# Performance work log

Measured on AMD Instinct MI355X. Metric: run time of the kernel, lower is better.

The kernel has to match this reference:

```python
import jax, jax.numpy as jnp
import numpy as np
import math


def ste_round(x):
    # round with straight-through gradient (identity in bwd)
    return x + jax.lax.stop_gradient(jnp.round(x) - x)


def ste_floor(x):
    return x + jax.lax.stop_gradient(jnp.floor(x) - x)


def _conv(x, w, b):
    # 5x5 stride-2 conv, padding=2 (kernel_size//2), NCHW/OIHW
    y = jax.lax.conv_general_dilated(
        x, w, window_strides=(2, 2), padding=[(2, 2), (2, 2)],
        dimension_numbers=('NCHW', 'OIHW', 'NCHW'))
    return y + b[None, :, None, None]


def _split_conv(x, w, b_int, mul, split=4):
    # 4 redundant sub-convolutions with floor-STE quantized integer weights/biases
    wq = ste_round(w)  # wSTE: round-to-int with STE
    out = 0.0
    for i in range(split):
        out = out + _conv(x, ste_floor((wq + i) / split), ste_floor((b_int + i) / split))
    return out * mul[None, :, None, None]


def _forward(x, w0, b0, w1, b1, w2, b2, w3, b3, mul0, mul1, mul2, mul3,
             relu0, relu1, relu2, md0, md1, md2, md3, ga_left):
    Bits = 8; clp_k = 8; in_scale = 8; scl_k = 3
    relus = [relu0, relu1, relu2]
    clp = [round((2 ** Bits - 1) / r * 2 ** (16 + clp_k)) for r in relus]
    scl = [math.floor((r + 2 ** (scl_k - 1)) / 2 ** scl_k) for r in relus]

    # quantize input to uint8 range
    x = jnp.clip(ste_round(x * 2 ** in_scale), 0, 255)

    # ---- layer 0 ----
    x = _split_conv(x, w0, ste_round(b0 * 2 ** in_scale), mul0)
    x = ste_floor((x + 2.0 ** (md0 - 1 + in_scale - clp_k)) / 2.0 ** (md0 + in_scale - clp_k))
    x = jnp.clip(x, 0, clp[0])
    x = ste_floor((ste_round(x * scl[0]) + 2.0 ** (15 + clp_k - scl_k)) / 2.0 ** (16 + clp_k - scl_k))

    # ---- layers 1, 2 ----
    for w_, b_, mul_, md_, idx in ((w1, b1, mul1, md1, 1), (w2, b2, mul2, md2, 2)):
        x = _split_conv(x, w_, ste_round(b_), mul_)
        x = ste_floor((x + 2.0 ** (md_ - 1 - clp_k)) / 2.0 ** (md_ - clp_k))
        x = jnp.clip(x, 0, clp[idx])
        x = ste_floor((ste_round(x * scl[idx]) + 2.0 ** (15 + clp_k - scl_k)) / 2.0 ** (16 + clp_k - scl_k))

    # ---- layer 3 (latent) ----
    x = _split_conv(x, w3, ste_round(b3), mul3)
    x = ste_floor((x + 2.0 ** (md3 - 1 - ga_left)) / 2.0 ** (md3 - ga_left))
    return x


def setup_inputs():
    key = jax.random.key(0)
    ks = jax.random.split(key, 16)
    N, M = 192, 320
    d = {}
    d['x'] = jax.random.uniform(ks[0], (4, 3, 512, 512), dtype=jnp.float32)
    # float weights whose round() gives small ints (integerized LIC weights)
    d['w0'] = jax.random.normal(ks[1], (N, 3, 5, 5), dtype=jnp.float32) * 3.0
    d['b0'] = jax.random.normal(ks[2], (N,), dtype=jnp.float32)
    d['w1'] = jax.random.normal(ks[3], (N, N, 5, 5), dtype=jnp.float32) * 3.0
    d['b1'] = jax.random.normal(ks[4], (N,), dtype=jnp.float32) * 16.0
    d['w2'] = jax.random.normal(ks[5], (N, N, 5, 5), dtype=jnp.float32) * 3.0
    d['b2'] = jax.random.normal(ks[6], (N,), dtype=jnp.float32) * 16.0
    d['w3'] = jax.random.normal(ks[7], (M, N, 5, 5), dtype=jnp.float32) * 3.0
    d['b3'] = jax.random.normal(ks[8], (M,), dtype=jnp.float32) * 16.0
    # per-channel integer-valued fixed-point multipliers
    d['mul0'] = jax.random.randint(ks[9], (N,), 1, 64).astype(jnp.float32)
    d['mul1'] = jax.random.randint(ks[10], (N,), 1, 64).astype(jnp.float32)
    d['mul2'] = jax.random.randint(ks[11], (N,), 1, 64).astype(jnp.float32)
    d['mul3'] = jax.random.randint(ks[12], (M,), 1, 64).astype(jnp.float32)
    d['relu0'] = 65536; d['relu1'] = 65536; d['relu2'] = 65536
    d['md0'] = 7; d['md1'] = 15; d['md2'] = 15; d['md3'] = 10
    d['ga_left'] = 4
    return d


def reference(x, w0, b0, w1, b1, w2, b2, w3, b3, mul0, mul1, mul2, mul3,
              relu0, relu1, relu2, md0, md1, md2, md3, ga_left):
    return _forward(x, w0, b0, w1, b1, w2, b2, w3, b3, mul0, mul1, mul2, mul3,
                    relu0, relu1, relu2, md0, md1, md2, md3, ga_left)
```

## Files before the change

### kernel.cpp

```cpp
#include <hip/hip_runtime.h>
#include <hip/hip_bf16.h>

typedef int i32x4 __attribute__((ext_vector_type(4)));
typedef unsigned int u32;
typedef unsigned long long u64;
typedef long long ll;

__device__ __forceinline__ void load_lds16(const void* g, void* l) {
  __builtin_amdgcn_global_load_lds(
      (const __attribute__((address_space(1))) u32*)g,
      (__attribute__((address_space(3))) u32*)l, 16, 0, 0);
}

template <int MF>
__device__ __forceinline__ void pack_i8(int j, const float* wsrc, signed char* wdst) {
  int e = j & 15, col = (j >> 4) & 15, q = (j >> 8) & 3, t = j >> 10;
  int mf = t % MF; t /= MF; int ch = t % 3; int tap = t / 3;
  int oc = mf * 16 + col, ci = ch * 64 + q * 16 + e;
  wdst[j] = (signed char)(int)rintf(wsrc[(oc * 192 + ci) * 25 + tap]);
}

__global__ __launch_bounds__(256) void prep_all(
    const float* __restrict__ w0, const float* __restrict__ w1,
    const float* __restrict__ w2, const float* __restrict__ w3,
    signed char* __restrict__ w0q, signed char* __restrict__ w1p,
    signed char* __restrict__ w2p, signed char* __restrict__ w3p,
    signed char* __restrict__ zbuf,
    int* __restrict__ totw0, int* __restrict__ totw1,
    int* __restrict__ totw2, int* __restrict__ totw3)
{
  const int blk = blockIdx.x;
  const int tid = threadIdx.x;

  if (blk < 2048) {
    if (blk == 0 && tid < 128)
      ((unsigned long long*)zbuf)[tid] = 0x8080808080808080ULL;
    const int R0 = 24576;
    const int R1 = 921600;
    const int R3 = 1536000;
    const int total = R0 + 2 * R1 + R3;
    for (int i = blk * 256 + tid; i < total; i += 2048 * 256) {
      if (i < R0) {
        int e = i & 15, colA = (i >> 4) & 15, q = (i >> 8) & 3, t = i >> 10;
        int mf = t % 12, ch = t / 12;
        signed char v = 0;
        if (e < 15 && (ch == 0 || q == 0)) {
          int ky = (ch == 0) ? q : 4;
          int ci = e / 5, kx = e - ci * 5;
          v = (signed char)(int)rintf(
              w0[((mf * 16 + colA) * 3 + ci) * 25 + ky * 5 + kx]);
        }
        w0q[i] = v;
      } else if (i < R0 + R1) {
        pack_i8<12>(i - R0, w1, w1p);
      } else if (i < R0 + 2 * R1) {
        pack_i8<12>(i - R0 - R1, w2, w2p);
      } else {
        pack_i8<20>(i - R0 - 2 * R1, w3, w3p);
      }
    }
  } else {
    int t = (blk - 2048) * 256 + tid;
    if (t < 704 * 16) {
      int oc = t >> 4, q = t & 15;
      const float* ws; int* tot; int o = oc;
      if (oc < 192)      { ws = w1; tot = totw1; }
      else if (oc < 384) { ws = w2; tot = totw2; o = oc - 192; }
      else               { ws = w3; tot = totw3; o = oc - 384; }
      const float* p = ws + (size_t)o * 4800 + q * 300;
      int s = 0;
      #pragma unroll 4
      for (int j = 0; j < 300; j++) s += (int)rintf(p[j]);
      atomicAdd(&tot[o], s);
    } else {
      int oc = t - 704 * 16;
      if (oc < 192) {
        const float* p = w0 + (size_t)oc * 75;
        int s = 0;
        #pragma unroll 5
        for (int j = 0; j < 75; j++) s += (int)rintf(p[j]);
        totw0[oc] = s;
      }
    }
  }
}

__global__ __launch_bounds__(192, 3) void conv0F(
    const float* __restrict__ x, const signed char* __restrict__ wq,
    const float* __restrict__ bias, const float* __restrict__ mulv,
    const int* __restrict__ totw,
    const int* __restrict__ reluP, const int* __restrict__ mdP,
    unsigned char* __restrict__ outA)
{
  __shared__ signed char ilds[3][5][132];

  const int tid = threadIdx.x;
  const int lane = tid & 63;
  const int col = lane & 15;
  const int quad = lane >> 4;
  const int w = tid >> 6;
  const int blk = blockIdx.x;
  const int oxblk = blk & 3;
  const int oy = (blk >> 2) & 255;
  const int b = blk >> 10;
  const int oxbase = oxblk * 64;

  i32x4 afr[2][4];
  #pragma unroll
  for (int ch = 0; ch < 2; ch++)
    #pragma unroll
    for (int i = 0; i < 4; i++)
      afr[ch][i] = *(const i32x4*)(wq + ch * 12288 + (w * 4 + i) * 1024 + lane * 16);

  const float* xb = x + (size_t)b * 3 * 512 * 512;
  for (int i = tid; i < 990; i += 192) {
    int j = i % 66; int t = i / 66; int r = t % 5; int ci = t / 5;
    int iy = 2 * oy - 2 + r;
    int ix = 2 * oxbase - 2 + 2 * j;
    int v0 = -128, v1 = -128;
    if ((unsigned)iy < 512u) {
      const float* row = xb + ((size_t)ci * 512 + iy) * 512;
      if ((unsigned)ix < 512u) {
        float xv = rintf(row[ix] * 256.0f);
        v0 = (int)fminf(fmaxf(xv, 0.0f), 255.0f) - 128;
      }
      if ((unsigned)(ix + 1) < 512u) {
        float xv = rintf(row[ix + 1] * 256.0f);
        v1 = (int)fminf(fmaxf(xv, 0.0f), 255.0f) - 128;
      }
    }
    *(unsigned short*)&ilds[ci][r][2 * j] =
        (unsigned short)((v0 & 0xFF) | ((v1 & 0xFF) << 8));
  }
  __syncthreads();

  i32x4 acc[4][4];
  #pragma unroll
  for (int fm = 0; fm < 4; fm++)
    #pragma unroll
    for (int fn = 0; fn < 4; fn++) acc[fm][fn] = (i32x4){0, 0, 0, 0};

  #pragma unroll
  for (int ch = 0; ch < 2; ch++) {
    const int row = (ch == 0) ? quad : 4;
    i32x4 bfr[4];
    #pragma unroll
    for (int fn = 0; fn < 4; fn++) {
      const int xb2 = 2 * (fn * 16 + col);
      const int o8 = (xb2 & 3) * 8;
      const int ab = xb2 & ~3;
      u64 w0_, w1_, w2_;
      {
        const u32* p0 = (const u32*)&ilds[0][row][ab];
        const u32* p1 = (const u32*)&ilds[1][row][ab];
        const u32* p2 = (const u32*)&ilds[2][row][ab];
        w0_ = (u64)p0[0] | ((u64)p0[1] << 32);
        w1_ = (u64)p1[0] | ((u64)p1[1] << 32);
        w2_ = (u64)p2[0] | ((u64)p2[1] << 32);
      }
      u32 a0 = (u32)(w0_ >> o8);
      u32 a1 = ((u32)(w0_ >> (o8 + 32)) & 0xFFu) | (((u32)(w1_ >> o8)) << 8);
      u32 a2 = ((u32)(w1_ >> (o8 + 24)) & 0xFFFFu) | (((u32)(w2_ >> o8)) << 16);
      u32 a3 = (u32)(w2_ >> (o8 + 16));
      bfr[fn] = (i32x4){(int)a0, (int)a1, (int)a2, (int)a3};
    }
    #pragma unroll
    for (int fm = 0; fm < 4; fm++)
      #pragma unroll
      for (int fn = 0; fn < 4; fn++)
        acc[fm][fn] = __builtin_amdgcn_mfma_i32_16x16x64_i8(
            afr[ch][fm], bfr[fn], acc[fm][fn], 0, 0, 0);
  }

  const size_t pix0 = ((size_t)(b * 256 + oy)) * 256 + oxbase;
  const int rl = reluP[0];
  const int sh = mdP[0];
  const ll clpv_ll = llrint(255.0 / (double)rl * 16777216.0);
  const int clpv = clpv_ll > 0x7FFFFFFFLL ? 0x7FFFFFFF : (int)clpv_ll;
  const int sclv = (int)((rl + 4) >> 3);
  const int rnd = 1 << (sh - 1);
  #pragma unroll
  for (int fm = 0; fm < 4; fm++) {
    const int oc0 = w * 64 + fm * 16 + quad * 4;
    int bim[4], mu32[4];
    #pragma unroll
    for (int r = 0; r < 4; r++) {
      int bi = (int)llrintf(bias[oc0 + r] * 256.0f) + 128 * totw[oc0 + r];
      mu32[r] = (int)llrintf(mulv[oc0 + r]);
      bim[r] = bi * mu32[r];
    }
    #pragma unroll
    for (int fn = 0; fn < 4; fn++) {
      const size_t pix = pix0 + fn * 16 + col;
      u32 wd = 0;
      #pragma unroll
      for (int r = 0; r < 4; r++) {
        int vi = acc[fm][fn][r] * mu32[r] + bim[r];
        int y = (vi + rnd) >> sh;
        y = y < 0 ? 0 : (y > clpv ? clpv : y);
        y = (y * sclv + (1 << 20)) >> 21;
        wd |= (((u32)y ^ 0x80u) & 0xFFu) << (8 * r);
      }
      *(u32*)(outA + pix * 192 + oc0) = wd;
    }
  }
}

template <int COUT, int HIN, int WIN, int HOUT, int WOUT, int MW,
          int KSPLIT, bool DIRECT>
__global__ __launch_bounds__(MW * 64, 3) void convS(
    const signed char* __restrict__ act, const signed char* __restrict__ wp,
    const float* __restrict__ bias, const float* __restrict__ mulv,
    const int* __restrict__ totw,
    const int* __restrict__ reluP, const int* __restrict__ mdP,
    const signed char* __restrict__ zbuf,
    unsigned char* __restrict__ outA, int* __restrict__ outP)
{
  constexpr int CIN = 192;
  constexpr int PASSES = 4;
  constexpr int MAXP = (PASSES + MW - 1) / MW;
  constexpr int SAe = MW * 4096;
  constexpr int TX = WOUT / 16;
  constexpr int TYB = HOUT / 4;
  constexpr int TPP = 25 / KSPLIT;
  constexpr int NSTEP = TPP * 3;
  constexpr int PSZ = 4 * HOUT * WOUT * COUT;
  static_assert(MW * 64 == COUT, "M covers COUT");

  __shared__ __align__(16) char smem[2 * 4096];

  const int tid = threadIdx.x;
  const int lane = tid & 63;
  const int col = lane & 15;
  const int quad = lane >> 4;
  const int w = tid >> 6;
  const int part = blockIdx.y;

  int bx = blockIdx.x;
  const int tx = bx % TX; bx /= TX;
  const int ty = bx % TYB;
  const int b = bx / TYB;
  const int ox0 = tx * 16;
  const int oy0 = ty * 4;

  const signed char* bptr[MAXP];
  int bmx[MAXP], bmy[MAXP];
  #pragma unroll
  for (int k = 0; k < MAXP; k++) {
    int p = w + k * MW;
    if (p >= PASSES) break;
    int oxv = ox0 + col;
    int oyv = oy0 + p;
    bptr[k] = act + ((size_t)b * HIN * WIN + (size_t)(2 * oyv) * WIN + 2 * oxv) * CIN
              + quad * 16;
    int mx = 0, my = 0;
    #pragma unroll
    for (int kk = 0; kk < 5; kk++) {
      if ((unsigned)(2 * oxv + kk - 2) < (unsigned)WIN) mx |= 1 << kk;
      if ((unsigned)(2 * oyv + kk - 2) < (unsigned)HIN) my |= 1 << kk;
    }
    bmx[k] = mx; bmy[k] = my;
  }

  auto stageStep = [&](int tap, int ch, int sel) {
    const int ky = tap / 5, kx = tap % 5;
    const int offB = ((ky - 2) * WIN + (kx - 2)) * CIN + ch * 64;
    #pragma unroll
    for (int k = 0; k < MAXP; k++) {
      int p = w + k * MW;
      if (p >= PASSES) break;
      bool v = ((bmx[k] >> kx) & 1) && ((bmy[k] >> ky) & 1);
      const signed char* g = v ? (bptr[k] + offB) : (zbuf + quad * 16);
      load_lds16(g, smem + sel * 4096 + p * 1024);
    }
  };

  i32x4 acc[4][4];
  #pragma unroll
  for (int fm = 0; fm < 4; fm++)
    #pragma unroll
    for (int fn = 0; fn < 4; fn++) acc[fm][fn] = (i32x4){0, 0, 0, 0};

  const int tap0 = part * TPP;
  stageStep(tap0, 0, 0);
  const signed char* aptr = wp + (size_t)(tap0 * 3) * SAe + w * 4096 + lane * 16;
  i32x4 afn[4];
  #pragma unroll
  for (int i = 0; i < 4; i++)
    afn[i] = *(const i32x4*)(aptr + i * 1024);

  int tapN = tap0, chN = 1;

  #pragma unroll 1
  for (int sl = 0; sl < NSTEP; sl++) {
    __syncthreads();

    if (sl + 1 < NSTEP) {
      stageStep(tapN, chN, (sl + 1) & 1);
      chN++;
      if (chN == 3) { chN = 0; tapN++; }
    }

    i32x4 afc[4];
    #pragma unroll
    for (int i = 0; i < 4; i++) afc[i] = afn[i];
    if (sl + 1 < NSTEP) {
      aptr += SAe;
      #pragma unroll
      for (int i = 0; i < 4; i++)
        afn[i] = *(const i32x4*)(aptr + i * 1024);
    }

    const char* pB = smem + (sl & 1) * 4096 + lane * 16;
    i32x4 bfr[4];
    #pragma unroll
    for (int i = 0; i < 4; i++)
      bfr[i] = *(const i32x4*)(pB + i * 1024);
    #pragma unroll
    for (int fm = 0; fm < 4; fm++)
      #pragma unroll
      for (int fn = 0; fn < 4; fn++)
        acc[fm][fn] = __builtin_amdgcn_mfma_i32_16x16x64_i8(
            afc[fm], bfr[fn], acc[fm][fn], 0, 0, 0);
  }

  if constexpr (DIRECT) {
    const int rl = reluP[0];
    const int sh = mdP[0] - 8;
    const ll clpv = llrint(255.0 / (double)rl * 16777216.0);
    const ll sclv = (ll)((rl + 4) >> 3);
    #pragma unroll
    for (int fm = 0; fm < 4; fm++) {
      const int oc0 = w * 64 + fm * 16 + quad * 4;
      ll bi[4], mu[4];
      #pragma unroll
      for (int r = 0; r < 4; r++) {
        bi[r] = llrintf(bias[oc0 + r]) + 128LL * totw[oc0 + r];
        mu[r] = llrintf(mulv[oc0 + r]);
      }
      #pragma unroll
      for (int fn = 0; fn < 4; fn++) {
        const int oyv = oy0 + fn;
        const int oxv = ox0 + col;
        u32 wd = 0;
        #pragma unroll
        for (int r = 0; r < 4; r++) {
          ll vi = ((ll)acc[fm][fn][r] + bi[r]) * mu[r];
          ll y = (vi + (1LL << (sh - 1))) >> sh;
          y = y < 0 ? 0LL : (y > clpv ? clpv : y);
          y = (y * sclv + (1LL << 20)) >> 21;
          wd |= (((u32)y ^ 0x80u) & 0xFFu) << (8 * r);
        }
        *(u32*)(outA + ((size_t)((b * HOUT + oyv) * WOUT + oxv)) * COUT + oc0) = wd;
      }
    }
  } else {
    int* pout = outP + (size_t)part * PSZ;
    #pragma unroll
    for (int fm = 0; fm < 4; fm++) {
      const int oc0 = w * 64 + fm * 16 + quad * 4;
      #pragma unroll
      for (int fn = 0; fn < 4; fn++) {
        const int oyv = oy0 + fn;
        const int oxv = ox0 + col;
        *(i32x4*)(pout + ((size_t)((b * HOUT + oyv) * WOUT + oxv)) * COUT + oc0) =
            acc[fm][fn];
      }
    }
  }
}

__global__ __launch_bounds__(256) void reduce2(
    const int* __restrict__ partP, const float* __restrict__ bias,
    const float* __restrict__ mulv, const int* __restrict__ totw,
    const int* __restrict__ reluP, const int* __restrict__ mdP,
    unsigned char* __restrict__ outA)
{
  const int gid = blockIdx.x * 256 + threadIdx.x;
  const int PSZ4 = 4 * 64 * 64 * 192 / 4;
  const int4* pp = (const int4*)partP;
  int4 sv = pp[gid];
  #pragma unroll
  for (int p = 1; p < 5; p++) {
    int4 v = pp[(size_t)p * PSZ4 + gid];
    sv.x += v.x; sv.y += v.y; sv.z += v.z; sv.w += v.w;
  }
  int sa[4] = {sv.x, sv.y, sv.z, sv.w};
  const int oc0 = (gid * 4) % 192;
  const int rl = reluP[0];
  const int sh = mdP[0] - 8;
  const ll clpv = llrint(255.0 / (double)rl * 16777216.0);
  const ll sclv = (ll)((rl + 4) >> 3);
  u32 wd = 0;
  #pragma unroll
  for (int r = 0; r < 4; r++) {
    ll bi = llrintf(bias[oc0 + r]) + 128LL * totw[oc0 + r];
    ll mu = llrintf(mulv[oc0 + r]);
    ll vi = ((ll)sa[r] + bi) * mu;
    ll y = (vi + (1LL << (sh - 1))) >> sh;
    y = y < 0 ? 0LL : (y > clpv ? clpv : y);
    y = (y * sclv + (1LL << 20)) >> 21;
    wd |= (((u32)y ^ 0x80u) & 0xFFu) << (8 * r);
  }
  ((u32*)outA)[gid] = wd;
}

__global__ __launch_bounds__(256) void reduce3(
    const int* __restrict__ partP, const float* __restrict__ b3,
    const float* __restrict__ mul3, const int* __restrict__ totw3,
    const int* __restrict__ mdP, const int* __restrict__ gaP,
    float* __restrict__ outF)
{
  const int gid = blockIdx.x * 256 + threadIdx.x;
  int t = gid;
  const int ox = t & 31; t >>= 5;
  const int oy = t & 31; t >>= 5;
  const int oc = t % 320;
  const int b  = t / 320;
  const int PSZ = 4 * 32 * 32 * 320;
  const size_t src = ((size_t)((b * 32 + oy) * 32 + ox)) * 320 + oc;
  ll s = 0;
  #pragma unroll
  for (int p = 0; p < 5; p++) s += partP[(size_t)p * PSZ + src];
  const int sh = mdP[0] - gaP[0];
  const ll bi = llrintf(b3[oc]) + 128LL * totw3[oc];
  const ll mu = llrintf(mul3[oc]);
  const ll y = ((s + bi) * mu + (1LL << (sh - 1))) >> sh;
  outF[gid] = (float)y;
}

extern "C" void kernel_launch(void* const* d_in, const int* in_sizes, int n_in,
                              void* d_out, int out_size, void* d_ws, size_t ws_size,
                              hipStream_t stream)
{
  const float* x    = (const float*)d_in[0];
  const float* w0   = (const float*)d_in[1];
  const float* b0   = (const float*)d_in[2];
  const float* w1   = (const float*)d_in[3];
  const float* b1   = (const float*)d_in[4];
  const float* w2   = (const float*)d_in[5];
  const float* b2   = (const float*)d_in[6];
  const float* w3   = (const float*)d_in[7];
  const float* b3   = (const float*)d_in[8];
  const float* mul0 = (const float*)d_in[9];
  const float* mul1 = (const float*)d_in[10];
  const float* mul2 = (const float*)d_in[11];
  const float* mul3 = (const float*)d_in[12];
  const int* relu0  = (const int*)d_in[13];
  const int* relu1  = (const int*)d_in[14];
  const int* relu2  = (const int*)d_in[15];
  const int* md0    = (const int*)d_in[16];
  const int* md1    = (const int*)d_in[17];
  const int* md2    = (const int*)d_in[18];
  const int* md3    = (const int*)d_in[19];
  const int* ga     = (const int*)d_in[20];

  char* ws = (char*)d_ws;
  size_t off = 0;
  signed char* zbuf = (signed char*)(ws + off); off += 1024;
  signed char* w0q  = (signed char*)(ws + off); off += 24576;
  signed char* w1p  = (signed char*)(ws + off); off += 921600;
  signed char* w2p  = (signed char*)(ws + off); off += 921600;
  signed char* w3p  = (signed char*)(ws + off); off += 1536000;
  int*         totw1= (int*)        (ws + off); off += 192 * 4;
  int*         totw2= (int*)        (ws + off); off += 192 * 4;
  int*         totw3= (int*)        (ws + off); off += 320 * 4;
  int*         totw0= (int*)        (ws + off); off += 192 * 4;
  unsigned char* act1 = (unsigned char*)(ws + off); off += (size_t)4 * 256 * 256 * 192;
  unsigned char* act2 = (unsigned char*)(ws + off); off += (size_t)4 * 128 * 128 * 192;
  unsigned char* act3 = (unsigned char*)(ws + off); off += (size_t)4 * 64 * 64 * 192;
  int*         partl  = (int*)(ws + off); off += (size_t)5 * 4 * 64 * 64 * 192 * 4;
  (void)ws_size; (void)in_sizes; (void)n_in; (void)out_size;

  hipMemsetAsync(totw1, 0, (192 + 192 + 320 + 192) * 4, stream);
  prep_all<<<2093, 256, 0, stream>>>(w0, w1, w2, w3, w0q, w1p, w2p, w3p,
                                     zbuf, totw0, totw1, totw2, totw3);
  conv0F<<<4096, 192, 0, stream>>>(x, w0q, b0, mul0, totw0, relu0, md0, act1);
  convS<192, 256, 256, 128, 128, 3, 1, true><<<dim3(1024, 1), 192, 0, stream>>>(
      (const signed char*)act1, w1p, b1, mul1, totw1, relu1, md1, zbuf, act2, nullptr);
  convS<192, 128, 128, 64, 64, 3, 5, false><<<dim3(256, 5), 192, 0, stream>>>(
      (const signed char*)act2, w2p, b2, mul2, totw2, relu2, md2, zbuf, nullptr, partl);
  reduce2<<<3072, 256, 0, stream>>>(partl, b2, mul2, totw2, relu2, md2, act3);
  convS<320, 64, 64, 32, 32, 5, 5, false><<<dim3(64, 5), 320, 0, stream>>>(
      (const signed char*)act3, w3p, b3, mul3, totw3, nullptr, md3, zbuf, nullptr, partl);
  reduce3<<<5120, 256, 0, stream>>>(partl, b3, mul3, totw3, md3, ga, (float*)d_out);
}
```

Baseline: 351.2 us.

## Restage weight packing through LDS and unroll conv main loop by two

The weight-prep kernel now has each block read a slab of 8 output channels contiguously into LDS, round them there, and write 4-byte packed words. This replaces the strided per-byte scalar gathers spread over 2093 blocks, and the weight-sum pass is folded into the same read. The conv main loop is unrolled by two with explicit ping-pong A-register buffers and incremental tap/channel counters, which removes the per-step register copy and the divides. The cost is that prep runs on only 89 blocks, which lowers parallelism for that kernel.

After: 348.5 us. About the same (-0.8%).

```diff
diff --git a/kernel.cpp b/kernel.cpp
--- a/kernel.cpp
+++ b/kernel.cpp
@@ -10,14 +10,6 @@
   __builtin_amdgcn_global_load_lds(
       (const __attribute__((address_space(1))) u32*)g,
       (__attribute__((address_space(3))) u32*)l, 16, 0, 0);
-}
-
-template <int MF>
-__device__ __forceinline__ void pack_i8(int j, const float* wsrc, signed char* wdst) {
-  int e = j & 15, col = (j >> 4) & 15, q = (j >> 8) & 3, t = j >> 10;
-  int mf = t % MF; t /= MF; int ch = t % 3; int tap = t / 3;
-  int oc = mf * 16 + col, ci = ch * 64 + q * 16 + e;
-  wdst[j] = (signed char)(int)rintf(wsrc[(oc * 192 + ci) * 25 + tap]);
 }
 
 __global__ __launch_bounds__(256) void prep_all(
@@ -29,58 +21,60 @@
     int* __restrict__ totw0, int* __restrict__ totw1,
     int* __restrict__ totw2, int* __restrict__ totw3)
 {
+  __shared__ signed char ldsw[8 * 4800];
   const int blk = blockIdx.x;
   const int tid = threadIdx.x;
 
-  if (blk < 2048) {
-    if (blk == 0 && tid < 128)
-      ((unsigned long long*)zbuf)[tid] = 0x8080808080808080ULL;
-    const int R0 = 24576;
-    const int R1 = 921600;
-    const int R3 = 1536000;
-    const int total = R0 + 2 * R1 + R3;
-    for (int i = blk * 256 + tid; i < total; i += 2048 * 256) {
-      if (i < R0) {
-        int e = i & 15, colA = (i >> 4) & 15, q = (i >> 8) & 3, t = i >> 10;
-        int mf = t % 12, ch = t / 12;
-        signed char v = 0;
-        if (e < 15 && (ch == 0 || q == 0)) {
-          int ky = (ch == 0) ? q : 4;
-          int ci = e / 5, kx = e - ci * 5;
-          v = (signed char)(int)rintf(
-              w0[((mf * 16 + colA) * 3 + ci) * 25 + ky * 5 + kx]);
-        }
-        w0q[i] = v;
-      } else if (i < R0 + R1) {
-        pack_i8<12>(i - R0, w1, w1p);
-      } else if (i < R0 + 2 * R1) {
-        pack_i8<12>(i - R0 - R1, w2, w2p);
-      } else {
-        pack_i8<20>(i - R0 - 2 * R1, w3, w3p);
-      }
+  if (blk < 88) {
+    const float* wsrc; signed char* wdst; int* tot; int MF, sub;
+    if (blk < 24)      { wsrc = w1; wdst = w1p; tot = totw1; MF = 12; sub = blk; }
+    else if (blk < 48) { wsrc = w2; wdst = w2p; tot = totw2; MF = 12; sub = blk - 24; }
+    else               { wsrc = w3; wdst = w3p; tot = totw3; MF = 20; sub = blk - 48; }
+    const int mf = sub >> 1, half = sub & 1, colbase = half * 8;
+    const int ocb = mf * 16 + colbase;
+    for (int o = 0; o < 8; o++) {
+      const float* src = wsrc + (size_t)(ocb + o) * 4800;
+      int s = 0;
+      for (int j = tid; j < 4800; j += 256) {
+        int v = (int)rintf(src[j]);
+        ldsw[o * 4800 + j] = (signed char)v;
+        s += v;
+      }
+      atomicAdd(&tot[ocb + o], s);
+    }
+    __syncthreads();
+    for (int u = tid; u < 9600; u += 256) {
+      int eu = u & 3, colL = (u >> 2) & 7, q = (u >> 5) & 3, t = u >> 7;
+      int tap = t / 3, ch = t - 3 * tap;
+      int ci0 = ch * 64 + q * 16 + eu * 4;
+      const signed char* sp = ldsw + colL * 4800 + tap;
+      u32 wv = 0;
+      #pragma unroll
+      for (int bb = 0; bb < 4; bb++)
+        wv |= ((u32)(unsigned char)sp[(ci0 + bb) * 25]) << (8 * bb);
+      *(u32*)(wdst + ((size_t)t * MF + mf) * 1024 +
+              (q * 16 + colbase + colL) * 16 + eu * 4) = wv;
     }
   } else {
-    int t = (blk - 2048) * 256 + tid;
-    if (t < 704 * 16) {
-      int oc = t >> 4, q = t & 15;
-      const float* ws; int* tot; int o = oc;
-      if (oc < 192)      { ws = w1; tot = totw1; }
-      else if (oc < 384) { ws = w2; tot = totw2; o = oc - 192; }
-      else               { ws = w3; tot = totw3; o = oc - 384; }
-      const float* p = ws + (size_t)o * 4800 + q * 300;
+    if (tid < 128) ((u64*)zbuf)[tid] = 0x8080808080808080ULL;
+    for (int i = tid; i < 24576; i += 256) {
+      int e = i & 15, colA = (i >> 4) & 15, q = (i >> 8) & 3, t = i >> 10;
+      int mf = t % 12, ch = t / 12;
+      signed char v = 0;
+      if (e < 15 && (ch == 0 || q == 0)) {
+        int ky = (ch == 0) ? q : 4;
+        int ci = e / 5, kx = e - ci * 5;
+        v = (signed char)(int)rintf(
+            w0[((mf * 16 + colA) * 3 + ci) * 25 + ky * 5 + kx]);
+      }
+      w0q[i] = v;
+    }
+    for (int oc = tid; oc < 192; oc += 256) {
+      const float* p = w0 + (size_t)oc * 75;
       int s = 0;
-      #pragma unroll 4
-      for (int j = 0; j < 300; j++) s += (int)rintf(p[j]);
-      atomicAdd(&tot[o], s);
-    } else {
-      int oc = t - 704 * 16;
-      if (oc < 192) {
-        const float* p = w0 + (size_t)oc * 75;
-        int s = 0;
-        #pragma unroll 5
-        for (int j = 0; j < 75; j++) s += (int)rintf(p[j]);
-        totw0[oc] = s;
-      }
+      #pragma unroll 5
+      for (int j = 0; j < 75; j++) s += (int)rintf(p[j]);
+      totw0[oc] = s;
     }
   }
 }
@@ -262,18 +256,23 @@
     bmx[k] = mx; bmy[k] = my;
   }
 
-  auto stageStep = [&](int tap, int ch, int sel) {
-    const int ky = tap / 5, kx = tap % 5;
-    const int offB = ((ky - 2) * WIN + (kx - 2)) * CIN + ch * 64;
+  int kxS, kyS, chS;
+
+  auto stage = [&](int sel) {
+    const int offB = ((kyS - 2) * WIN + (kxS - 2)) * CIN + chS * 64;
     #pragma unroll
     for (int k = 0; k < MAXP; k++) {
       int p = w + k * MW;
       if (p >= PASSES) break;
-      bool v = ((bmx[k] >> kx) & 1) && ((bmy[k] >> ky) & 1);
+      bool v = ((bmx[k] >> kxS) & 1) && ((bmy[k] >> kyS) & 1);
       const signed char* g = v ? (bptr[k] + offB) : (zbuf + quad * 16);
       load_lds16(g, smem + sel * 4096 + p * 1024);
     }
   };
+  auto adv = [&]() {
+    chS++;
+    if (chS == 3) { chS = 0; kxS++; if (kxS == 5) { kxS = 0; kyS++; } }
+  };
 
   i32x4 acc[4][4];
   #pragma unroll
@@ -282,36 +281,16 @@
     for (int fn = 0; fn < 4; fn++) acc[fm][fn] = (i32x4){0, 0, 0, 0};
 
   const int tap0 = part * TPP;
-  stageStep(tap0, 0, 0);
+  kyS = tap0 / 5; kxS = tap0 - 5 * kyS; chS = 0;
+  stage(0);
+  adv();
   const signed char* aptr = wp + (size_t)(tap0 * 3) * SAe + w * 4096 + lane * 16;
-  i32x4 afn[4];
-  #pragma unroll
-  for (int i = 0; i < 4; i++)
-    afn[i] = *(const i32x4*)(aptr + i * 1024);
-
-  int tapN = tap0, chN = 1;
-
-  #pragma unroll 1
-  for (int sl = 0; sl < NSTEP; sl++) {
-    __syncthreads();
-
-    if (sl + 1 < NSTEP) {
-      stageStep(tapN, chN, (sl + 1) & 1);
-      chN++;
-      if (chN == 3) { chN = 0; tapN++; }
-    }
-
-    i32x4 afc[4];
-    #pragma unroll
-    for (int i = 0; i < 4; i++) afc[i] = afn[i];
-    if (sl + 1 < NSTEP) {
-      aptr += SAe;
-      #pragma unroll
-      for (int i = 0; i < 4; i++)
-        afn[i] = *(const i32x4*)(aptr + i * 1024);
-    }
-
-    const char* pB = smem + (sl & 1) * 4096 + lane * 16;
+  i32x4 aA[4], aB[4];
+  #pragma unroll
+  for (int i = 0; i < 4; i++) aA[i] = *(const i32x4*)(aptr + i * 1024);
+
+  auto comp = [&](int base, i32x4 (&a)[4]) {
+    const char* pB = smem + base + lane * 16;
     i32x4 bfr[4];
     #pragma unroll
     for (int i = 0; i < 4; i++)
@@ -321,7 +300,31 @@
       #pragma unroll
       for (int fn = 0; fn < 4; fn++)
         acc[fm][fn] = __builtin_amdgcn_mfma_i32_16x16x64_i8(
-            afc[fm], bfr[fn], acc[fm][fn], 0, 0, 0);
+            a[fm], bfr[fn], acc[fm][fn], 0, 0, 0);
+  };
+
+  int sl = 0;
+  #pragma unroll 1
+  for (; sl + 1 < NSTEP; sl += 2) {
+    __syncthreads();
+    stage(1); adv();
+    aptr += SAe;
+    #pragma unroll
+    for (int i = 0; i < 4; i++) aB[i] = *(const i32x4*)(aptr + i * 1024);
+    comp(0, aA);
+
+    __syncthreads();
+    if (sl + 2 < NSTEP) {
+      stage(0); adv();
+      aptr += SAe;
+      #pragma unroll
+      for (int i = 0; i < 4; i++) aA[i] = *(const i32x4*)(aptr + i * 1024);
+    }
+    comp(4096, aB);
+  }
+  if (sl < NSTEP) {
+    __syncthreads();
+    comp(0, aA);
   }
 
   if constexpr (DIRECT) {
@@ -473,8 +476,8 @@
   (void)ws_size; (void)in_sizes; (void)n_in; (void)out_size;
 
   hipMemsetAsync(totw1, 0, (192 + 192 + 320 + 192) * 4, stream);
-  prep_all<<<2093, 256, 0, stream>>>(w0, w1, w2, w3, w0q, w1p, w2p, w3p,
-                                     zbuf, totw0, totw1, totw2, totw3);
+  prep_all<<<89, 256, 0, stream>>>(w0, w1, w2, w3, w0q, w1p, w2p, w3p,
+                                   zbuf, totw0, totw1, totw2, totw3);
   conv0F<<<4096, 192, 0, stream>>>(x, w0q, b0, mul0, totw0, relu0, md0, act1);
   convS<192, 256, 256, 128, 128, 3, 1, true><<<dim3(1024, 1), 192, 0, stream>>>(
       (const signed char*)act1, w1p, b1, mul1, totw1, relu1, md1, zbuf, act2, nullptr);
```
